# Kernel optimization log

Hardware: AMD Instinct MI355X
Metric: run time of the kernel (lower is better)

The kernel has to match this reference:

```python
import jax, jax.numpy as jnp
import numpy as np

B, N, P, D = 32, 128, 8, 512


def setup_inputs() -> dict:
    key = jax.random.key(0)
    k_x, k_w1, k_b1, k_w2, k_b2 = jax.random.split(key, 5)
    lim = 1.0 / np.sqrt(D)  # torch Linear init range
    x = jax.random.normal(k_x, (B, N, P, D), dtype=jnp.float32)
    # torch Linear weights are [out, in]; stack per-patch -> [P, D, D]
    W1 = jax.random.uniform(k_w1, (P, D, D), minval=-lim, maxval=lim, dtype=jnp.float32)
    b1 = jax.random.uniform(k_b1, (P, D), minval=-lim, maxval=lim, dtype=jnp.float32)
    W2 = jax.random.uniform(k_w2, (P, D, D), minval=-lim, maxval=lim, dtype=jnp.float32)
    b2 = jax.random.uniform(k_b2, (P, D), minval=-lim, maxval=lim, dtype=jnp.float32)
    return {"x": x, "W1": W1, "b1": b1, "W2": W2, "b2": b2}


def reference(x, W1, b1, W2, b2):
    # Per-patch 2-layer MLP with GELU, batched as one grouped GEMM pair.
    # torch Linear: y = x @ W.T + b  ->  einsum over 'kd' with W[p, k, d]
    h = jnp.einsum('bnpd,pkd->bnpk', x, W1) + b1  # [B, N, P, D]
    h = jax.nn.gelu(h, approximate=False)          # nn.GELU default is exact
    o = jnp.einsum('bnpd,pkd->bnpk', h, W2) + b2  # [B, N, P, D]
    # Dropout p=0.0 -> identity. Residual add.
    return o + x
```

## Files before the change

kernel.cpp:

```cpp
#include <hip/hip_runtime.h>
#include <stdint.h>


typedef unsigned short u16;
typedef __attribute__((ext_vector_type(8))) short bf16x8;
typedef __attribute__((ext_vector_type(4))) float f32x4;

#define AS1 __attribute__((address_space(1)))
#define AS3 __attribute__((address_space(3)))

#define MTOT 4096
#define PATCHES 8
#define DDIM 512
#define ROWSTRIDE 4096

__device__ __forceinline__ void glds16(const void* g, void* l) {
  __builtin_amdgcn_global_load_lds((const AS1 uint32_t*)g, (AS3 uint32_t*)l, 16, 0, 0);
}

__device__ __forceinline__ u16 bf16_rne(float v) {
  union { float f; uint32_t u; } c; c.f = v;
  uint32_t u = c.u + 0x7FFFu + ((c.u >> 16) & 1u);
  return (u16)(u >> 16);
}
__device__ __forceinline__ float bf16_to_f(u16 h) {
  union { uint32_t u; float f; } c; c.u = ((uint32_t)h) << 16;
  return c.f;
}
__device__ __forceinline__ void split2(float v, u16& hi, u16& lo) {
  hi = bf16_rne(v);
  float r = v - bf16_to_f(hi);
  lo = bf16_rne(r);
}

__global__ void split_kernel(const float* __restrict__ in,
                             u16* __restrict__ hi, u16* __restrict__ lo, int n) {
  int i = (blockIdx.x * blockDim.x + threadIdx.x) * 4;
  int stride = gridDim.x * blockDim.x * 4;
  for (; i < n; i += stride) {
    float4 v = *reinterpret_cast<const float4*>(in + i);
    ushort4 h, l;
    split2(v.x, h.x, l.x);
    split2(v.y, h.y, l.y);
    split2(v.z, h.z, l.z);
    split2(v.w, h.w, l.w);
    *reinterpret_cast<ushort4*>(hi + i) = h;
    *reinterpret_cast<ushort4*>(lo + i) = l;
  }
}

template <int EPI>
__global__ __launch_bounds__(256) void gemm_split(
    const u16* __restrict__ Ahi, const u16* __restrict__ Alo,
    const u16* __restrict__ Bhi, const u16* __restrict__ Blo,
    const float* __restrict__ bias,
    const float* __restrict__ resid,
    u16* __restrict__ OutHi, u16* __restrict__ OutLo,
    float* __restrict__ OutF)
{
  const int nwg = gridDim.x;
  const int bid = blockIdx.x;
  const int swz = (bid & 7) * (nwg >> 3) + (bid >> 3);
  const int nt = swz & 3;
  const int mt = (swz >> 2) & 31;
  const int p  = swz >> 7;

  __shared__ __attribute__((aligned(16))) u16 lsAhi[128 * 32];
  __shared__ __attribute__((aligned(16))) u16 lsAlo[128 * 32];
  __shared__ __attribute__((aligned(16))) u16 lsBhi[128 * 32];
  __shared__ __attribute__((aligned(16))) u16 lsBlo[128 * 32];

  const int tid = threadIdx.x;
  const int lane = tid & 63;
  const int wv = tid >> 6;
  const int wr = wv >> 1;
  const int wc = wv & 1;
  const int fr = lane & 15;
  const int fk = (lane >> 4) * 8;

  const int e0 = tid * 8;
  const int r0 = e0 >> 5;
  const int c0 = e0 & 31;
  const size_t aBase  = (size_t)(mt * 128 + r0) * ROWSTRIDE + (size_t)p * DDIM + c0;
  const size_t aBase1 = aBase + (size_t)64 * ROWSTRIDE;
  const size_t bBase  = (size_t)p * (DDIM * DDIM) + (size_t)(nt * 128 + r0) * DDIM + c0;
  const size_t bBase1 = bBase + (size_t)64 * DDIM;

  f32x4 acc[4][4] = {};

  for (int kt = 0; kt < 16; ++kt) {
    const int ko = kt * 32;
    glds16(Ahi + aBase  + ko, &lsAhi[e0]);
    glds16(Ahi + aBase1 + ko, &lsAhi[e0 + 2048]);
    glds16(Alo + aBase  + ko, &lsAlo[e0]);
    glds16(Alo + aBase1 + ko, &lsAlo[e0 + 2048]);
    glds16(Bhi + bBase  + ko, &lsBhi[e0]);
    glds16(Bhi + bBase1 + ko, &lsBhi[e0 + 2048]);
    glds16(Blo + bBase  + ko, &lsBlo[e0]);
    glds16(Blo + bBase1 + ko, &lsBlo[e0 + 2048]);
    __syncthreads();

    bf16x8 ah[4], al[4], bh[4], bl[4];
#pragma unroll
    for (int i = 0; i < 4; ++i) {
      const int ra = (wr * 64 + i * 16 + fr) * 32 + fk;
      const int rb = (wc * 64 + i * 16 + fr) * 32 + fk;
      ah[i] = *(const bf16x8*)&lsAhi[ra];
      al[i] = *(const bf16x8*)&lsAlo[ra];
      bh[i] = *(const bf16x8*)&lsBhi[rb];
      bl[i] = *(const bf16x8*)&lsBlo[rb];
    }
#pragma unroll
    for (int i = 0; i < 4; ++i) {
#pragma unroll
      for (int j = 0; j < 4; ++j) {
        acc[i][j] = __builtin_amdgcn_mfma_f32_16x16x32_bf16(ah[i], bh[j], acc[i][j], 0, 0, 0);
        acc[i][j] = __builtin_amdgcn_mfma_f32_16x16x32_bf16(al[i], bh[j], acc[i][j], 0, 0, 0);
        acc[i][j] = __builtin_amdgcn_mfma_f32_16x16x32_bf16(ah[i], bl[j], acc[i][j], 0, 0, 0);
      }
    }
    __syncthreads();
  }

  const int rquad = (lane >> 4) * 4;
#pragma unroll
  for (int j = 0; j < 4; ++j) {
    const int col = nt * 128 + wc * 64 + j * 16 + fr;
    const float bj = bias[p * DDIM + col];
#pragma unroll
    for (int i = 0; i < 4; ++i) {
      const int row = mt * 128 + wr * 64 + i * 16 + rquad;
#pragma unroll
      for (int r = 0; r < 4; ++r) {
        const size_t idx = (size_t)(row + r) * ROWSTRIDE + (size_t)p * DDIM + col;
        float o = acc[i][j][r] + bj;
        if constexpr (EPI == 1) {
          o = 0.5f * o * (1.0f + erff(o * 0.70710678118654752f));
          u16 h_, l_;
          split2(o, h_, l_);
          OutHi[idx] = h_;
          OutLo[idx] = l_;
        } else {
          OutF[idx] = o + resid[idx];
        }
      }
    }
  }
}

extern "C" void kernel_launch(void* const* d_in, const int* in_sizes, int n_in,
                              void* d_out, int out_size, void* d_ws, size_t ws_size,
                              hipStream_t stream) {
  const float* x  = (const float*)d_in[0];
  const float* W1 = (const float*)d_in[1];
  const float* b1 = (const float*)d_in[2];
  const float* W2 = (const float*)d_in[3];
  const float* b2 = (const float*)d_in[4];
  float* out = (float*)d_out;

  const int NX = MTOT * PATCHES * DDIM;
  const int NW = PATCHES * DDIM * DDIM;

  u16* ws   = (u16*)d_ws;
  u16* xhi  = ws;
  u16* xlo  = xhi + NX;
  u16* w1hi = xlo + NX;
  u16* w1lo = w1hi + NW;
  u16* w2hi = w1lo + NW;
  u16* w2lo = w2hi + NW;
  u16* hhi  = w2lo + NW;
  u16* hlo  = hhi + NX;

  split_kernel<<<2048, 256, 0, stream>>>(x,  xhi,  xlo,  NX);
  split_kernel<<<512,  256, 0, stream>>>(W1, w1hi, w1lo, NW);
  split_kernel<<<512,  256, 0, stream>>>(W2, w2hi, w2lo, NW);

  gemm_split<1><<<1024, 256, 0, stream>>>(xhi, xlo, w1hi, w1lo, b1, nullptr,
                                          hhi, hlo, nullptr);
  gemm_split<2><<<1024, 256, 0, stream>>>(hhi, hlo, w2hi, w2lo, b2, x,
                                          nullptr, nullptr, out);
}
```

Before: 301.5 us.

## Use 256x256 tiles with double-buffered LDS, swizzle, and fused split kernel

Both split-bf16 GEMMs move from 128x128 tiles with 4 waves to 256x256 tiles with 8 waves and double-buffered LDS. The next k-step's global-to-LDS loads are spread across four phases of the MFMA loop, with barriers and setprio around each phase. An XOR swizzle on LDS columns reduces bank conflicts, and the three split launches are merged into one kernel. The aim is to hide memory latency and raise MFMA utilisation. In exchange, 128KB of LDS and more registers per block cut occupancy, and the grid drops to 256 blocks, so fewer workgroups run concurrently.

```diff
diff --git a/kernel.cpp b/kernel.cpp
--- a/kernel.cpp
+++ b/kernel.cpp
@@ -33,24 +33,30 @@
   lo = bf16_rne(r);
 }
 
-__global__ void split_kernel(const float* __restrict__ in,
-                             u16* __restrict__ hi, u16* __restrict__ lo, int n) {
-  int i = (blockIdx.x * blockDim.x + threadIdx.x) * 4;
-  int stride = gridDim.x * blockDim.x * 4;
-  for (; i < n; i += stride) {
-    float4 v = *reinterpret_cast<const float4*>(in + i);
-    ushort4 h, l;
-    split2(v.x, h.x, l.x);
-    split2(v.y, h.y, l.y);
-    split2(v.z, h.z, l.z);
-    split2(v.w, h.w, l.w);
-    *reinterpret_cast<ushort4*>(hi + i) = h;
-    *reinterpret_cast<ushort4*>(lo + i) = l;
+__global__ void split3_kernel(const float* __restrict__ x,  u16* xhi,  u16* xlo,  int nx,
+                              const float* __restrict__ w1, u16* w1hi, u16* w1lo,
+                              const float* __restrict__ w2, u16* w2hi, u16* w2lo, int nw) {
+  const int total4 = (nx + 2 * nw) >> 2;
+  for (int i4 = blockIdx.x * blockDim.x + threadIdx.x; i4 < total4;
+       i4 += gridDim.x * blockDim.x) {
+    int i = i4 << 2;
+    const float* src; u16* h; u16* l; int off;
+    if (i < nx)           { src = x;  h = xhi;  l = xlo;  off = i; }
+    else if (i < nx + nw) { src = w1; h = w1hi; l = w1lo; off = i - nx; }
+    else                  { src = w2; h = w2hi; l = w2lo; off = i - nx - nw; }
+    float4 v = *reinterpret_cast<const float4*>(src + off);
+    ushort4 hh, ll;
+    split2(v.x, hh.x, ll.x);
+    split2(v.y, hh.y, ll.y);
+    split2(v.z, hh.z, ll.z);
+    split2(v.w, hh.w, ll.w);
+    *reinterpret_cast<ushort4*>(h + off) = hh;
+    *reinterpret_cast<ushort4*>(l + off) = ll;
   }
 }
 
 template <int EPI>
-__global__ __launch_bounds__(256) void gemm_split(
+__global__ __launch_bounds__(512, 2) void gemm_split8(
     const u16* __restrict__ Ahi, const u16* __restrict__ Alo,
     const u16* __restrict__ Bhi, const u16* __restrict__ Blo,
     const float* __restrict__ bias,
@@ -61,75 +67,125 @@
   const int nwg = gridDim.x;
   const int bid = blockIdx.x;
   const int swz = (bid & 7) * (nwg >> 3) + (bid >> 3);
-  const int nt = swz & 3;
-  const int mt = (swz >> 2) & 31;
-  const int p  = swz >> 7;
-
-  __shared__ __attribute__((aligned(16))) u16 lsAhi[128 * 32];
-  __shared__ __attribute__((aligned(16))) u16 lsAlo[128 * 32];
-  __shared__ __attribute__((aligned(16))) u16 lsBhi[128 * 32];
-  __shared__ __attribute__((aligned(16))) u16 lsBlo[128 * 32];
-
-  const int tid = threadIdx.x;
-  const int lane = tid & 63;
-  const int wv = tid >> 6;
-  const int wr = wv >> 1;
-  const int wc = wv & 1;
-  const int fr = lane & 15;
-  const int fk = (lane >> 4) * 8;
-
-  const int e0 = tid * 8;
-  const int r0 = e0 >> 5;
-  const int c0 = e0 & 31;
-  const size_t aBase  = (size_t)(mt * 128 + r0) * ROWSTRIDE + (size_t)p * DDIM + c0;
-  const size_t aBase1 = aBase + (size_t)64 * ROWSTRIDE;
-  const size_t bBase  = (size_t)p * (DDIM * DDIM) + (size_t)(nt * 128 + r0) * DDIM + c0;
-  const size_t bBase1 = bBase + (size_t)64 * DDIM;
-
-  f32x4 acc[4][4] = {};
+  const int nt = swz & 1;
+  const int mt = (swz >> 1) & 15;
+  const int p  = swz >> 5;
+
+  __shared__ __attribute__((aligned(16))) u16 sm[2][4][256 * 32];
+
+  const int t    = threadIdx.x;
+  const int lane = t & 63;
+  const int wv   = t >> 6;
+  const int wr   = wv >> 2;
+  const int wc   = wv & 3;
+  const int fr   = lane & 15;
+  const int cS   = (lane >> 4) ^ ((fr >> 1) & 3);
+
+  const int sr0 = t >> 2;
+  const int sc  = t & 3;
+  const int scS = sc ^ ((sr0 >> 1) & 3);
+  const int se0 = t * 8;
+  const int se1 = se0 + 4096;
+
+  const size_t aG0 = (size_t)(mt * 256 + sr0)       * ROWSTRIDE + (size_t)p * DDIM + scS * 8;
+  const size_t aG1 = (size_t)(mt * 256 + sr0 + 128) * ROWSTRIDE + (size_t)p * DDIM + scS * 8;
+  const size_t bG0 = ((size_t)p * DDIM + nt * 256 + sr0)       * DDIM + scS * 8;
+  const size_t bG1 = ((size_t)p * DDIM + nt * 256 + sr0 + 128) * DDIM + scS * 8;
+
+  f32x4 acc[8][4] = {};
+
+  glds16(Ahi + aG0, &sm[0][0][se0]); glds16(Ahi + aG1, &sm[0][0][se1]);
+  glds16(Alo + aG0, &sm[0][1][se0]); glds16(Alo + aG1, &sm[0][1][se1]);
+  glds16(Bhi + bG0, &sm[0][2][se0]); glds16(Bhi + bG1, &sm[0][2][se1]);
+  glds16(Blo + bG0, &sm[0][3][se0]); glds16(Blo + bG1, &sm[0][3][se1]);
+  asm volatile("s_waitcnt vmcnt(0)" ::: "memory");
+  __builtin_amdgcn_s_barrier();
+
+#define DS_A(pl, m) (*(const bf16x8*)&sm[cur][pl][(wr * 128 + (m) * 16 + fr) * 32 + cS * 8])
+#define DS_B(pl, n) (*(const bf16x8*)&sm[cur][pl][(wc * 64  + (n) * 16 + fr) * 32 + cS * 8])
+#define MFMA3(m, a_h, a_l)                                                            \
+  _Pragma("unroll")                                                                   \
+  for (int n = 0; n < 4; ++n) {                                                       \
+    acc[m][n] = __builtin_amdgcn_mfma_f32_16x16x32_bf16(a_h, bh[n], acc[m][n], 0,0,0);\
+    acc[m][n] = __builtin_amdgcn_mfma_f32_16x16x32_bf16(a_l, bh[n], acc[m][n], 0,0,0);\
+    acc[m][n] = __builtin_amdgcn_mfma_f32_16x16x32_bf16(a_h, bl[n], acc[m][n], 0,0,0);\
+  }
 
   for (int kt = 0; kt < 16; ++kt) {
-    const int ko = kt * 32;
-    glds16(Ahi + aBase  + ko, &lsAhi[e0]);
-    glds16(Ahi + aBase1 + ko, &lsAhi[e0 + 2048]);
-    glds16(Alo + aBase  + ko, &lsAlo[e0]);
-    glds16(Alo + aBase1 + ko, &lsAlo[e0 + 2048]);
-    glds16(Bhi + bBase  + ko, &lsBhi[e0]);
-    glds16(Bhi + bBase1 + ko, &lsBhi[e0 + 2048]);
-    glds16(Blo + bBase  + ko, &lsBlo[e0]);
-    glds16(Blo + bBase1 + ko, &lsBlo[e0 + 2048]);
-    __syncthreads();
-
-    bf16x8 ah[4], al[4], bh[4], bl[4];
-#pragma unroll
-    for (int i = 0; i < 4; ++i) {
-      const int ra = (wr * 64 + i * 16 + fr) * 32 + fk;
-      const int rb = (wc * 64 + i * 16 + fr) * 32 + fk;
-      ah[i] = *(const bf16x8*)&lsAhi[ra];
-      al[i] = *(const bf16x8*)&lsAlo[ra];
-      bh[i] = *(const bf16x8*)&lsBhi[rb];
-      bl[i] = *(const bf16x8*)&lsBlo[rb];
-    }
-#pragma unroll
-    for (int i = 0; i < 4; ++i) {
-#pragma unroll
-      for (int j = 0; j < 4; ++j) {
-        acc[i][j] = __builtin_amdgcn_mfma_f32_16x16x32_bf16(ah[i], bh[j], acc[i][j], 0, 0, 0);
-        acc[i][j] = __builtin_amdgcn_mfma_f32_16x16x32_bf16(al[i], bh[j], acc[i][j], 0, 0, 0);
-        acc[i][j] = __builtin_amdgcn_mfma_f32_16x16x32_bf16(ah[i], bl[j], acc[i][j], 0, 0, 0);
-      }
-    }
-    __syncthreads();
-  }
+    const int cur = kt & 1, nxt = cur ^ 1;
+    const bool stage = (kt != 15);
+    const size_t ko = (size_t)(kt + 1) * 32;
+
+    bf16x8 bh[4], bl[4];
+
+    {
+#pragma unroll
+      for (int n = 0; n < 4; ++n) { bh[n] = DS_B(2, n); bl[n] = DS_B(3, n); }
+      bf16x8 a0h = DS_A(0, 0), a1h = DS_A(0, 1);
+      bf16x8 a0l = DS_A(1, 0), a1l = DS_A(1, 1);
+      if (stage) { glds16(Ahi + aG0 + ko, &sm[nxt][0][se0]);
+                   glds16(Ahi + aG1 + ko, &sm[nxt][0][se1]); }
+      __builtin_amdgcn_s_barrier();
+      asm volatile("s_waitcnt lgkmcnt(0)" ::: "memory");
+      __builtin_amdgcn_s_setprio(1);
+      MFMA3(0, a0h, a0l)
+      MFMA3(1, a1h, a1l)
+      __builtin_amdgcn_s_setprio(0);
+      __builtin_amdgcn_s_barrier();
+    }
+    {
+      bf16x8 a0h = DS_A(0, 2), a1h = DS_A(0, 3);
+      bf16x8 a0l = DS_A(1, 2), a1l = DS_A(1, 3);
+      if (stage) { glds16(Alo + aG0 + ko, &sm[nxt][1][se0]);
+                   glds16(Alo + aG1 + ko, &sm[nxt][1][se1]); }
+      __builtin_amdgcn_s_barrier();
+      asm volatile("s_waitcnt lgkmcnt(0)" ::: "memory");
+      __builtin_amdgcn_s_setprio(1);
+      MFMA3(2, a0h, a0l)
+      MFMA3(3, a1h, a1l)
+      __builtin_amdgcn_s_setprio(0);
+      __builtin_amdgcn_s_barrier();
+    }
+    {
+      bf16x8 a0h = DS_A(0, 4), a1h = DS_A(0, 5);
+      bf16x8 a0l = DS_A(1, 4), a1l = DS_A(1, 5);
+      if (stage) { glds16(Bhi + bG0 + ko, &sm[nxt][2][se0]);
+                   glds16(Bhi + bG1 + ko, &sm[nxt][2][se1]); }
+      __builtin_amdgcn_s_barrier();
+      asm volatile("s_waitcnt lgkmcnt(0)" ::: "memory");
+      __builtin_amdgcn_s_setprio(1);
+      MFMA3(4, a0h, a0l)
+      MFMA3(5, a1h, a1l)
+      __builtin_amdgcn_s_setprio(0);
+      __builtin_amdgcn_s_barrier();
+    }
+    {
+      bf16x8 a0h = DS_A(0, 6), a1h = DS_A(0, 7);
+      bf16x8 a0l = DS_A(1, 6), a1l = DS_A(1, 7);
+      if (stage) { glds16(Blo + bG0 + ko, &sm[nxt][3][se0]);
+                   glds16(Blo + bG1 + ko, &sm[nxt][3][se1]); }
+      __builtin_amdgcn_s_barrier();
+      asm volatile("s_waitcnt lgkmcnt(0)" ::: "memory");
+      __builtin_amdgcn_s_setprio(1);
+      MFMA3(6, a0h, a0l)
+      MFMA3(7, a1h, a1l)
+      __builtin_amdgcn_s_setprio(0);
+      asm volatile("s_waitcnt vmcnt(0)" ::: "memory");
+      __builtin_amdgcn_s_barrier();
+    }
+  }
+#undef DS_A
+#undef DS_B
+#undef MFMA3
 
   const int rquad = (lane >> 4) * 4;
 #pragma unroll
   for (int j = 0; j < 4; ++j) {
-    const int col = nt * 128 + wc * 64 + j * 16 + fr;
+    const int col = nt * 256 + wc * 64 + j * 16 + fr;
     const float bj = bias[p * DDIM + col];
 #pragma unroll
-    for (int i = 0; i < 4; ++i) {
-      const int row = mt * 128 + wr * 64 + i * 16 + rquad;
+    for (int i = 0; i < 8; ++i) {
+      const int row = mt * 256 + wr * 128 + i * 16 + rquad;
 #pragma unroll
       for (int r = 0; r < 4; ++r) {
         const size_t idx = (size_t)(row + r) * ROWSTRIDE + (size_t)p * DDIM + col;
@@ -171,12 +227,12 @@
   u16* hhi  = w2lo + NW;
   u16* hlo  = hhi + NX;
 
-  split_kernel<<<2048, 256, 0, stream>>>(x,  xhi,  xlo,  NX);
-  split_kernel<<<512,  256, 0, stream>>>(W1, w1hi, w1lo, NW);
-  split_kernel<<<512,  256, 0, stream>>>(W2, w2hi, w2lo, NW);
-
-  gemm_split<1><<<1024, 256, 0, stream>>>(xhi, xlo, w1hi, w1lo, b1, nullptr,
+  split3_kernel<<<2048, 256, 0, stream>>>(x, xhi, xlo, NX,
+                                          W1, w1hi, w1lo,
+                                          W2, w2hi, w2lo, NW);
+
+  gemm_split8<1><<<256, 512, 0, stream>>>(xhi, xlo, w1hi, w1lo, b1, nullptr,
                                           hhi, hlo, nullptr);
-  gemm_split<2><<<1024, 256, 0, stream>>>(hhi, hlo, w2hi, w2lo, b2, x,
+  gemm_split8<2><<<256, 512, 0, stream>>>(hhi, hlo, w2hi, w2lo, b2, x,
                                           nullptr, nullptr, out);
 }
```

New measurement: 297.4 us. Within noise of the previous version (-1.4%).
